# Kernel tuning notes

Measured on AMD Instinct MI355X. Metric: run time of the kernel, lower is better.

Reference implementation:

```python
import jax, jax.numpy as jnp
import numpy as np


def setup_inputs() -> dict:
    key = jax.random.key(0)
    k1, k2 = jax.random.split(key)
    L, B, C, H, W = 4, 8, 256, 64, 64
    inputs = jax.random.normal(k1, (L, B, C, H, W), dtype=jnp.float32)
    # nn.Linear(C, C, bias=False) weight: [out, in]
    Wlin = jax.random.normal(k2, (C, C), dtype=jnp.float32) * (1.0 / np.sqrt(C))
    return {"inputs": inputs, "W": Wlin}


def reference(inputs, W):
    # inputs: [L, B, C, H, W] -- stacked input_list; W: [C, C] linear weight
    # GAP over spatial dims -> [L, B, C]
    gap = jnp.mean(inputs, axis=(3, 4))
    # torch Linear: y = x @ W^T  -> scores [L, B, C]
    scores = jnp.einsum('lbc,dc->lbd', gap, W)
    # original loops over channels doing softmax over the layer axis;
    # vectorized: softmax across L for each (b, c)
    attn = jax.nn.softmax(scores, axis=0)  # [L, B, C]
    # broadcast multiply each level by its per-channel attention
    out = inputs * attn[:, :, :, None, None]
    return out
```

## Files before the change

### kernel.cpp

```cpp
#include <hip/hip_runtime.h>
#include <stdint.h>


#define L_DIM 4
#define B_DIM 8
#define C_DIM 256
#define HW    4096
#define F4_PER_CH (HW / 4)
#define NCH   (L_DIM * B_DIM * C_DIM)
#define NBD   (B_DIM * C_DIM)

typedef float nfloat4 __attribute__((ext_vector_type(4)));

__global__ __launch_bounds__(256) void gap_kernel(
        const float4* __restrict__ in, float* __restrict__ gap) {
    const int ch = blockIdx.x;
    const float4* base = in + (size_t)ch * F4_PER_CH;
    float s = 0.0f;
    #pragma unroll
    for (int k = 0; k < 4; ++k) {
        float4 p = base[threadIdx.x + k * 256];
        s += (p.x + p.y) + (p.z + p.w);
    }
    #pragma unroll
    for (int off = 32; off > 0; off >>= 1)
        s += __shfl_down(s, off, 64);
    __shared__ float wsum[4];
    const int wave = threadIdx.x >> 6;
    const int lane = threadIdx.x & 63;
    if (lane == 0) wsum[wave] = s;
    __syncthreads();
    if (threadIdx.x == 0) {
        gap[ch] = (wsum[0] + wsum[1] + wsum[2] + wsum[3]) * (1.0f / (float)HW);
    }
}

__global__ __launch_bounds__(256) void attn_kernel(
        const float* __restrict__ gap, const float* __restrict__ Wf,
        float* __restrict__ attn) {
    const int bid = blockIdx.x;
    const int d   = bid & (C_DIM - 1);
    const int b   = bid >> 8;
    const int c   = threadIdx.x;

    const float w = Wf[(size_t)d * C_DIM + c];
    float p0 = gap[(0 * B_DIM + b) * C_DIM + c] * w;
    float p1 = gap[(1 * B_DIM + b) * C_DIM + c] * w;
    float p2 = gap[(2 * B_DIM + b) * C_DIM + c] * w;
    float p3 = gap[(3 * B_DIM + b) * C_DIM + c] * w;

    #pragma unroll
    for (int off = 32; off > 0; off >>= 1) {
        p0 += __shfl_down(p0, off, 64);
        p1 += __shfl_down(p1, off, 64);
        p2 += __shfl_down(p2, off, 64);
        p3 += __shfl_down(p3, off, 64);
    }
    __shared__ float part[4][4];
    const int wave = threadIdx.x >> 6;
    const int lane = threadIdx.x & 63;
    if (lane == 0) {
        part[wave][0] = p0; part[wave][1] = p1;
        part[wave][2] = p2; part[wave][3] = p3;
    }
    __syncthreads();
    if (threadIdx.x < 4) {
        const float s0 = part[0][0] + part[1][0] + part[2][0] + part[3][0];
        const float s1 = part[0][1] + part[1][1] + part[2][1] + part[3][1];
        const float s2 = part[0][2] + part[1][2] + part[2][2] + part[3][2];
        const float s3 = part[0][3] + part[1][3] + part[2][3] + part[3][3];
        const float m  = fmaxf(fmaxf(s0, s1), fmaxf(s2, s3));
        const float e0 = __expf(s0 - m), e1 = __expf(s1 - m);
        const float e2 = __expf(s2 - m), e3 = __expf(s3 - m);
        const float inv = 1.0f / (e0 + e1 + e2 + e3);
        const int   l   = threadIdx.x;
        const float el  = (l == 0) ? e0 : (l == 1) ? e1 : (l == 2) ? e2 : e3;
        attn[(l * B_DIM + b) * C_DIM + d] = el * inv;
    }
}

__global__ __launch_bounds__(256) void scale_kernel(
        const float4* __restrict__ in, const float* __restrict__ attn,
        float4* __restrict__ out) {
    const int ch = blockIdx.x;
    const float a = attn[ch];
    const float4* src = in + (size_t)ch * F4_PER_CH;
    nfloat4*      dst = (nfloat4*)(out + (size_t)ch * F4_PER_CH);
    #pragma unroll
    for (int k = 0; k < 4; ++k) {
        float4 p = src[threadIdx.x + k * 256];
        nfloat4 q = { p.x * a, p.y * a, p.z * a, p.w * a };
        __builtin_nontemporal_store(q, &dst[threadIdx.x + k * 256]);
    }
}

extern "C" void kernel_launch(void* const* d_in, const int* in_sizes, int n_in,
                              void* d_out, int out_size, void* d_ws, size_t ws_size,
                              hipStream_t stream) {
    const float4* in_p  = (const float4*)d_in[0];
    const float*  W_p   = (const float*)d_in[1];
    float4*       out_p = (float4*)d_out;

    float* gap  = (float*)d_ws;
    float* attn = (float*)d_ws + NCH;

    gap_kernel  <<<NCH, 256, 0, stream>>>(in_p, gap);
    attn_kernel <<<NBD, 256, 0, stream>>>(gap, W_p, attn);
    scale_kernel<<<NCH, 256, 0, stream>>>(in_p, attn, out_p);
}
```

Baseline: 248.8 us.

## Fuse GAP, attention and scaling into one persistent kernel with grid barrier

Replaces the three kernels with a single persistent kernel of 1024 blocks. Each block first computes the spatial means for its (b,d) pairs across all four levels, then waits at a software grid-wide barrier built on an atomic counter. After the barrier it computes the softmax attention for its pairs and scales the same channels it reduced earlier. This removes two kernel launches and the attention round trip through global memory, and the second read of each block's data may hit in cache. The cost is a spin barrier that needs all 1024 blocks to be resident at once, plus an extra memset before each launch.

```diff
diff --git a/kernel.cpp b/kernel.cpp
--- a/kernel.cpp
+++ b/kernel.cpp
@@ -8,89 +8,102 @@
 #define HW    4096
 #define F4_PER_CH (HW / 4)
 #define NCH   (L_DIM * B_DIM * C_DIM)
-#define NBD   (B_DIM * C_DIM)
+#define GRID_BLOCKS 1024
+#define PAIRS 2
 
 typedef float nfloat4 __attribute__((ext_vector_type(4)));
 
-__global__ __launch_bounds__(256) void gap_kernel(
-        const float4* __restrict__ in, float* __restrict__ gap) {
-    const int ch = blockIdx.x;
-    const float4* base = in + (size_t)ch * F4_PER_CH;
-    float s = 0.0f;
-    #pragma unroll
-    for (int k = 0; k < 4; ++k) {
-        float4 p = base[threadIdx.x + k * 256];
-        s += (p.x + p.y) + (p.z + p.w);
-    }
-    #pragma unroll
-    for (int off = 32; off > 0; off >>= 1)
-        s += __shfl_down(s, off, 64);
-    __shared__ float wsum[4];
-    const int wave = threadIdx.x >> 6;
-    const int lane = threadIdx.x & 63;
-    if (lane == 0) wsum[wave] = s;
-    __syncthreads();
-    if (threadIdx.x == 0) {
-        gap[ch] = (wsum[0] + wsum[1] + wsum[2] + wsum[3]) * (1.0f / (float)HW);
-    }
-}
-
-__global__ __launch_bounds__(256) void attn_kernel(
-        const float* __restrict__ gap, const float* __restrict__ Wf,
-        float* __restrict__ attn) {
-    const int bid = blockIdx.x;
-    const int d   = bid & (C_DIM - 1);
-    const int b   = bid >> 8;
-    const int c   = threadIdx.x;
-
-    const float w = Wf[(size_t)d * C_DIM + c];
-    float p0 = gap[(0 * B_DIM + b) * C_DIM + c] * w;
-    float p1 = gap[(1 * B_DIM + b) * C_DIM + c] * w;
-    float p2 = gap[(2 * B_DIM + b) * C_DIM + c] * w;
-    float p3 = gap[(3 * B_DIM + b) * C_DIM + c] * w;
+__global__ __launch_bounds__(256, 4) void sffm_fused(
+        const float4* __restrict__ in, const float* __restrict__ Wf,
+        float* __restrict__ gap, unsigned* __restrict__ bar,
+        float4* __restrict__ out) {
+    const int t    = threadIdx.x;
+    const int wave = t >> 6;
+    const int lane = t & 63;
 
     #pragma unroll
-    for (int off = 32; off > 0; off >>= 1) {
-        p0 += __shfl_down(p0, off, 64);
-        p1 += __shfl_down(p1, off, 64);
-        p2 += __shfl_down(p2, off, 64);
-        p3 += __shfl_down(p3, off, 64);
+    for (int p = 0; p < PAIRS; ++p) {
+        const int bid = blockIdx.x * PAIRS + p;
+        const int d   = bid & (C_DIM - 1);
+        const int b   = bid >> 8;
+        const int ch  = ((wave * B_DIM + b) << 8) + d;
+        const float4* base = in + (size_t)ch * F4_PER_CH;
+        float s = 0.0f;
+        #pragma unroll
+        for (int k = 0; k < 16; ++k) {
+            float4 v = base[lane + k * 64];
+            s += (v.x + v.y) + (v.z + v.w);
+        }
+        #pragma unroll
+        for (int off = 32; off > 0; off >>= 1)
+            s += __shfl_down(s, off, 64);
+        if (lane == 0) gap[ch] = s * (1.0f / (float)HW);
     }
-    __shared__ float part[4][4];
-    const int wave = threadIdx.x >> 6;
-    const int lane = threadIdx.x & 63;
-    if (lane == 0) {
-        part[wave][0] = p0; part[wave][1] = p1;
-        part[wave][2] = p2; part[wave][3] = p3;
+
+    __syncthreads();
+    if (t == 0) {
+        __threadfence();
+        __hip_atomic_fetch_add(bar, 1u, __ATOMIC_RELAXED,
+                               __HIP_MEMORY_SCOPE_AGENT);
+        while (__hip_atomic_load(bar, __ATOMIC_RELAXED,
+                                 __HIP_MEMORY_SCOPE_AGENT) < GRID_BLOCKS) {}
+        __threadfence();
     }
     __syncthreads();
-    if (threadIdx.x < 4) {
-        const float s0 = part[0][0] + part[1][0] + part[2][0] + part[3][0];
-        const float s1 = part[0][1] + part[1][1] + part[2][1] + part[3][1];
-        const float s2 = part[0][2] + part[1][2] + part[2][2] + part[3][2];
-        const float s3 = part[0][3] + part[1][3] + part[2][3] + part[3][3];
-        const float m  = fmaxf(fmaxf(s0, s1), fmaxf(s2, s3));
-        const float e0 = __expf(s0 - m), e1 = __expf(s1 - m);
-        const float e2 = __expf(s2 - m), e3 = __expf(s3 - m);
-        const float inv = 1.0f / (e0 + e1 + e2 + e3);
-        const int   l   = threadIdx.x;
-        const float el  = (l == 0) ? e0 : (l == 1) ? e1 : (l == 2) ? e2 : e3;
-        attn[(l * B_DIM + b) * C_DIM + d] = el * inv;
-    }
-}
 
-__global__ __launch_bounds__(256) void scale_kernel(
-        const float4* __restrict__ in, const float* __restrict__ attn,
-        float4* __restrict__ out) {
-    const int ch = blockIdx.x;
-    const float a = attn[ch];
-    const float4* src = in + (size_t)ch * F4_PER_CH;
-    nfloat4*      dst = (nfloat4*)(out + (size_t)ch * F4_PER_CH);
-    #pragma unroll
-    for (int k = 0; k < 4; ++k) {
-        float4 p = src[threadIdx.x + k * 256];
-        nfloat4 q = { p.x * a, p.y * a, p.z * a, p.w * a };
-        __builtin_nontemporal_store(q, &dst[threadIdx.x + k * 256]);
+    __shared__ float part[4][4];
+    __shared__ float a_s[4];
+
+    for (int p = 0; p < PAIRS; ++p) {
+        const int bid = blockIdx.x * PAIRS + p;
+        const int d   = bid & (C_DIM - 1);
+        const int b   = bid >> 8;
+
+        const float wv = Wf[(size_t)d * C_DIM + t];
+        float p0 = gap[(0 * B_DIM + b) * C_DIM + t] * wv;
+        float p1 = gap[(1 * B_DIM + b) * C_DIM + t] * wv;
+        float p2 = gap[(2 * B_DIM + b) * C_DIM + t] * wv;
+        float p3 = gap[(3 * B_DIM + b) * C_DIM + t] * wv;
+        #pragma unroll
+        for (int off = 32; off > 0; off >>= 1) {
+            p0 += __shfl_down(p0, off, 64);
+            p1 += __shfl_down(p1, off, 64);
+            p2 += __shfl_down(p2, off, 64);
+            p3 += __shfl_down(p3, off, 64);
+        }
+        if (lane == 0) {
+            part[wave][0] = p0; part[wave][1] = p1;
+            part[wave][2] = p2; part[wave][3] = p3;
+        }
+        __syncthreads();
+        if (t < 4) {
+            const float s0 = part[0][0] + part[1][0] + part[2][0] + part[3][0];
+            const float s1 = part[0][1] + part[1][1] + part[2][1] + part[3][1];
+            const float s2 = part[0][2] + part[1][2] + part[2][2] + part[3][2];
+            const float s3 = part[0][3] + part[1][3] + part[2][3] + part[3][3];
+            const float m  = fmaxf(fmaxf(s0, s1), fmaxf(s2, s3));
+            const float e0 = __expf(s0 - m), e1 = __expf(s1 - m);
+            const float e2 = __expf(s2 - m), e3 = __expf(s3 - m);
+            const float inv = 1.0f / (e0 + e1 + e2 + e3);
+            const float el  = (t == 0) ? e0 : (t == 1) ? e1 : (t == 2) ? e2 : e3;
+            a_s[t] = el * inv;
+        }
+        __syncthreads();
+        const float a0 = a_s[0], a1 = a_s[1], a2 = a_s[2], a3 = a_s[3];
+
+        #pragma unroll
+        for (int l = 0; l < L_DIM; ++l) {
+            const float a = (l == 0) ? a0 : (l == 1) ? a1 : (l == 2) ? a2 : a3;
+            const int ch = ((l * B_DIM + b) << 8) + d;
+            const float4* src = in + (size_t)ch * F4_PER_CH;
+            nfloat4*      dst = (nfloat4*)(out + (size_t)ch * F4_PER_CH);
+            #pragma unroll
+            for (int k = 0; k < 4; ++k) {
+                float4 v = src[t + k * 256];
+                nfloat4 q = { v.x * a, v.y * a, v.z * a, v.w * a };
+                __builtin_nontemporal_store(q, &dst[t + k * 256]);
+            }
+        }
     }
 }
 
@@ -100,11 +113,10 @@
     const float4* in_p  = (const float4*)d_in[0];
     const float*  W_p   = (const float*)d_in[1];
     float4*       out_p = (float4*)d_out;
+    float*        gap   = (float*)d_ws;
+    unsigned*     bar   = (unsigned*)((char*)d_ws + NCH * sizeof(float));
 
-    float* gap  = (float*)d_ws;
-    float* attn = (float*)d_ws + NCH;
+    hipMemsetAsync((void*)bar, 0, sizeof(unsigned), stream);
 
-    gap_kernel  <<<NCH, 256, 0, stream>>>(in_p, gap);
-    attn_kernel <<<NBD, 256, 0, stream>>>(gap, W_p, attn);
-    scale_kernel<<<NCH, 256, 0, stream>>>(in_p, attn, out_p);
+    sffm_fused<<<GRID_BLOCKS, 256, 0, stream>>>(in_p, W_p, gap, bar, out_p);
 }
```

Result: slower. 372.6 us (+49.7%).
